# Performance work log

Hardware: AMD Instinct MI355X
Metric: run time of the kernel (lower is better)

Reference implementation:

```python
import jax, jax.numpy as jnp
import numpy as np

B, T, C, J = 2048, 128, 3, 25   # batch, frames, coords, joints
E = 64                          # structure elements (n_elements)


def setup_inputs() -> dict:
    key = jax.random.key(0)
    k1, k2 = jax.random.split(key)
    x = jax.random.normal(k1, (B, T, C, J), dtype=jnp.float32)
    centres = jax.random.uniform(k2, (E, 2), dtype=jnp.float32)
    sharpness = jnp.full((E, 2), 3.0, dtype=jnp.float32)  # torch init: ones*3
    return {"x": x, "centres": centres, "sharpness": sharpness}


def _mst_deaths(Dm):
    """Prim's MST over dense distance matrix Dm [n,n].
    The multiset of MST edge weights equals the finite death times of the
    0-dim Vietoris-Rips persistence diagram (births are all 0)."""
    n = Dm.shape[0]
    in_tree0 = jnp.zeros(n, dtype=bool).at[0].set(True)

    def step(carry, _):
        mind, in_tree = carry
        masked = jnp.where(in_tree, jnp.inf, mind)  # distance from tree to each node
        j = jnp.argmin(masked)
        w = masked[j]                               # weight of edge added to MST
        in_tree = in_tree.at[j].set(True)
        mind = jnp.minimum(mind, Dm[j])
        return (mind, in_tree), w

    (_, _), deaths = jax.lax.scan(step, (Dm[0], in_tree0), None, length=n - 1)
    return deaths  # [n-1]


def reference(x, centres, sharpness):
    # --- dense preprocessing ---
    h = x.mean(1)                           # [B, C, J]
    h = h[..., :, None] - h[..., None, :]   # [B, C, J, J] pairwise coord diffs
    h = h.mean(-3)                          # [B, J, J]
    h = jnp.sqrt((h * h).sum(axis=1))       # torch.norm(., 2, dim=1) -> [B, J]
    lo, hi = h.min(), h.max()
    rng = hi - lo
    safe = rng > 1e-8
    h = jnp.where(safe, (h - lo) / jnp.where(safe, rng, 1.0), jnp.zeros_like(h))

    # --- Vietoris-Rips dim-0 persistence on point cloud h: B points in J dims ---
    sq = (h * h).sum(-1)
    d2 = sq[:, None] + sq[None, :] - 2.0 * (h @ h.T)       # [B, B]
    Dm = jnp.sqrt(jnp.maximum(d2, 1e-12))
    deaths = _mst_deaths(Dm)                               # [B-1]
    pd = jnp.stack([jnp.zeros_like(deaths), deaths], -1)[None]  # [1, P, 2]

    # --- StructureElementLayer: out[b,e] = sum_p exp(-sum_d s[e,d]^2 (pd-c)^2) ---
    s2 = sharpness * sharpness                             # [E, 2]
    diff = pd[:, :, None, :] - centres[None, None, :, :]   # [1, P, E, 2]
    out = jnp.exp(-(diff * diff * s2).sum(-1)).sum(1)      # [1, E]
    return out
```

## Files before the change

kernel.cpp:

```cpp
#include <hip/hip_runtime.h>
#include <math.h>

#define B_N 2048
#define T_N 128
#define C_N 3
#define J_N 25
#define E_N 64
#define TC  (T_N*C_N)
#define TCJ (TC*J_N)
#define NQ4 (TCJ/4)
#define NC  256

#define D_OFF      0
#define H_OFF      (B_N*B_N)
#define BLO_OFF    (H_OFF + B_N*J_N)
#define BHI_OFF    (BLO_OFF + B_N)
#define DEATHS_OFF (BHI_OFF + B_N)
#define BEST_OFF   (DEATHS_OFF + B_N)
#define COMP_OFF   (BEST_OFF + 4*B_N)
#define GC_OFF     (COMP_OFF + 2*B_N)
#define DC_OFF     (GC_OFF + 2)

typedef unsigned long long u64;
#define U64MAX 0xFFFFFFFFFFFFFFFFull
#define U32INF 0xFFFFFFFFu

__global__ void __launch_bounds__(256) k_reduce(const float* __restrict__ x,
                                                float* __restrict__ ws) {
    __shared__ float4 part[250];
    __shared__ float S[100];
    __shared__ float Mj[25];
    const int t = threadIdx.x, b = blockIdx.x;
    const float4* x4 = (const float4*)(x + (size_t)b * TCJ);
    if (t < 250) {
        float4 a; a.x = a.y = a.z = a.w = 0.f;
        for (int idx = t; idx < NQ4; idx += 250) {
            float4 v = x4[idx];
            a.x += v.x; a.y += v.y; a.z += v.z; a.w += v.w;
        }
        part[t] = a;
    }
    __syncthreads();
    if (t < 25) {
        float4 s = part[t];
        #pragma unroll
        for (int g = 1; g < 10; ++g) {
            float4 v = part[t + 25 * g];
            s.x += v.x; s.y += v.y; s.z += v.z; s.w += v.w;
        }
        S[4*t] = s.x; S[4*t+1] = s.y; S[4*t+2] = s.z; S[4*t+3] = s.w;
    }
    __syncthreads();
    if (t < 25) Mj[t] = (S[t] + S[t+25] + S[t+50] + S[t+75]) * (1.0f / 384.0f);
    __syncthreads();
    if (t < 25) {
        float mj = Mj[t], acc = 0.f;
        #pragma unroll
        for (int i = 0; i < J_N; ++i) { float d = Mj[i] - mj; acc += d * d; }
        float hv = sqrtf(acc);
        ws[H_OFF + b * J_N + t] = hv;
        S[t] = hv;
    }
    __syncthreads();
    if (t == 0) {
        float lo = S[0], hi = S[0];
        #pragma unroll
        for (int i = 1; i < J_N; ++i) { lo = fminf(lo, S[i]); hi = fmaxf(hi, S[i]); }
        ws[BLO_OFF + b] = lo;
        ws[BHI_OFF + b] = hi;
    }
}

__global__ void __launch_bounds__(1024) k_distscan(float* __restrict__ ws) {
    __shared__ float A[8][26];
    __shared__ float Bsh[1024 * J_N];
    __shared__ u64 part[16];
    const int t = threadIdx.x, blk = blockIdx.x;
    const int tx = t & 127, grp = t >> 7;
    const float* h = ws + H_OFF;
    const int row0 = blk * 8;
    if (t < 8 * J_N) A[t / J_N][t % J_N] = h[row0 * J_N + t];
    if (blk < 64) ((unsigned*)(ws + DC_OFF))[blk * 1024 + t] = U32INF;
    if (blk == 0) {
        unsigned* gc = (unsigned*)(ws + COMP_OFF);
        gc[t] = (unsigned)t; gc[t + 1024] = (unsigned)(t + 1024);
        if (t == 0) { ((unsigned*)(ws + GC_OFF))[0] = 0u; ((unsigned*)(ws + GC_OFF))[1] = 0u; }
    }
    const int row = row0 + grp;
    float ar[J_N];
    u64 bestk = U64MAX;
    float* D = ws + D_OFF;
    for (int mt = 0; mt < 2; ++mt) {
        __syncthreads();
        for (int idx = t; idx < 1024 * J_N; idx += 1024)
            Bsh[idx] = h[mt * 1024 * J_N + idx];
        __syncthreads();
        if (mt == 0) {
            #pragma unroll
            for (int k = 0; k < J_N; ++k) ar[k] = A[grp][k];
        }
        #pragma unroll 2
        for (int cc = 0; cc < 8; ++cc) {
            const int lcol = cc * 128 + tx;
            const int col = mt * 1024 + lcol;
            const float* bp = &Bsh[lcol * J_N];
            float acc = 0.f;
            #pragma unroll
            for (int k = 0; k < J_N; ++k) { float d = ar[k] - bp[k]; acc += d * d; }
            float dist = sqrtf(fmaxf(acc, 1e-12f));
            D[(size_t)row * B_N + col] = dist;
            if (col != row) {
                unsigned a = min((unsigned)row, (unsigned)col);
                unsigned b2 = max((unsigned)row, (unsigned)col);
                u64 key = ((u64)__float_as_uint(dist) << 32) | (a << 11) | b2;
                if (key < bestk) bestk = key;
            }
        }
    }
    #pragma unroll
    for (int off = 32; off; off >>= 1) {
        u64 o = __shfl_down(bestk, off);
        if (o < bestk) bestk = o;
    }
    if ((t & 63) == 0) part[t >> 6] = bestk;
    __syncthreads();
    if (t < 8) {
        u64 a = part[2 * t], b = part[2 * t + 1];
        ((u64*)(ws + BEST_OFF))[row0 + t] = a < b ? a : b;
    }
}

__global__ void __launch_bounds__(1024) k_round(float* __restrict__ ws, int par_in) {
    unsigned* gcnt = (unsigned*)(ws + GC_OFF);
    const unsigned base = gcnt[par_in];
    if (base >= B_N - 1) return;
    __shared__ __align__(16) unsigned comp[B_N];
    __shared__ u64 cb[B_N];
    __shared__ unsigned par[B_N];
    __shared__ unsigned cnt_s;
    const int t = threadIdx.x, blk = blockIdx.x;
    const unsigned* gcomp_in = (const unsigned*)(ws + COMP_OFF) + par_in * B_N;
    unsigned* gcomp_out = (unsigned*)(ws + COMP_OFF) + (par_in ^ 1) * B_N;
    const u64* bin = (const u64*)(ws + BEST_OFF) + par_in * B_N;
    u64* bout = (u64*)(ws + BEST_OFF) + (par_in ^ 1) * B_N;
    float* deaths = ws + DEATHS_OFF;

    if (t == 0) cnt_s = 0u;
    comp[t] = gcomp_in[t]; comp[t + 1024] = gcomp_in[t + 1024];
    cb[t] = U64MAX; cb[t + 1024] = U64MAX;
    __syncthreads();
    #pragma unroll
    for (int i = t; i < B_N; i += 1024) {
        u64 bk = bin[i];
        if (bk != U64MAX) atomicMin(&cb[comp[i]], bk);
    }
    __syncthreads();
    #pragma unroll
    for (int c = t; c < B_N; c += 1024) {
        u64 k = cb[c];
        unsigned p = (unsigned)c;
        if (k != U64MAX) {
            unsigned a  = (unsigned)((k >> 11) & 0x7FFu);
            unsigned b2 = (unsigned)(k & 0x7FFu);
            unsigned ca = comp[a], cbv = comp[b2];
            unsigned c2 = (ca == (unsigned)c) ? cbv : ca;
            p = c2;
            if (!(cb[c2] == k && c2 < (unsigned)c)) {
                unsigned li = atomicAdd(&cnt_s, 1u);
                if (blk == 0) deaths[base + li] = __uint_as_float((unsigned)(k >> 32));
            }
        }
        par[c] = p;
    }
    __syncthreads();
    #pragma unroll
    for (int c = t; c < B_N; c += 1024) {
        unsigned p = par[c];
        if (p != (unsigned)c && par[p] == (unsigned)c && (unsigned)c < p) par[c] = (unsigned)c;
    }
    __syncthreads();
    #pragma unroll
    for (int c = t; c < B_N; c += 1024) {
        unsigned r = par[c];
        while (true) { unsigned pr = par[r]; if (pr == r) break; r = pr; }
        par[c] = r;
    }
    __syncthreads();
    #pragma unroll
    for (int i = t; i < B_N; i += 1024) comp[i] = par[comp[i]];
    __syncthreads();
    const unsigned newbase = base + cnt_s;
    if (blk == 0) {
        gcomp_out[t] = comp[t]; gcomp_out[t + 1024] = comp[t + 1024];
        if (t == 0) { gcnt[par_in ^ 1] = newbase; if (newbase >= B_N - 1) gcnt[par_in] = newbase; }
    }
    if (newbase >= B_N - 1) return;

    const int w = t >> 6, lane = t & 63;
    if (w >= 8) return;
    const int row = blk * 8 + w;
    const unsigned ci = comp[row];
    u64 prev = bin[row];
    {
        unsigned pa = (unsigned)((prev >> 11) & 0x7FFu);
        unsigned pb = (unsigned)(prev & 0x7FFu);
        unsigned jo = (pa == (unsigned)row) ? pb : pa;
        if (comp[jo] != ci) {
            if (lane == 0) bout[row] = prev;
            return;
        }
    }
    const float4* row4 = (const float4*)(ws + D_OFF + (size_t)row * B_N);
    const uint4* comp4 = (const uint4*)comp;
    u64 best = U64MAX;
    #pragma unroll
    for (int k = 0; k < 8; ++k) {
        const int q = k * 64 + lane;
        float4 w4 = row4[q];
        uint4  c4 = comp4[q];
        const unsigned j0 = (unsigned)(q * 4);
        float wv[4] = {w4.x, w4.y, w4.z, w4.w};
        unsigned cv[4] = {c4.x, c4.y, c4.z, c4.w};
        #pragma unroll
        for (int m = 0; m < 4; ++m) {
            if (cv[m] != ci) {
                unsigned j = j0 + m;
                unsigned a = min((unsigned)row, j), b2 = max((unsigned)row, j);
                u64 key = ((u64)__float_as_uint(wv[m]) << 32) | (a << 11) | b2;
                if (key < best) best = key;
            }
        }
    }
    #pragma unroll
    for (int off = 32; off; off >>= 1) {
        u64 o = __shfl_down(best, off);
        if (o < best) best = o;
    }
    if (lane == 0) bout[row] = best;
}

__global__ void __launch_bounds__(1024) k_round3c(float* __restrict__ ws) {
    unsigned* gcnt = (unsigned*)(ws + GC_OFF);
    const unsigned base = gcnt[0];
    if (base >= B_N - 1) return;
    __shared__ __align__(16) unsigned comp[B_N];
    __shared__ u64 cb[B_N];
    __shared__ unsigned par[B_N];
    __shared__ unsigned cflag[B_N];
    __shared__ unsigned pd[8][NC];
    __shared__ unsigned cnt_s, csum[16];
    const int t = threadIdx.x, blk = blockIdx.x;
    const unsigned* gcomp_in = (const unsigned*)(ws + COMP_OFF);
    const u64* bin = (const u64*)(ws + BEST_OFF);
    float* deaths = ws + DEATHS_OFF;

    if (t == 0) cnt_s = 0u;
    comp[t] = gcomp_in[t]; comp[t + 1024] = gcomp_in[t + 1024];
    cb[t] = U64MAX; cb[t + 1024] = U64MAX;
    __syncthreads();
    #pragma unroll
    for (int i = t; i < B_N; i += 1024) {
        u64 bk = bin[i];
        if (bk != U64MAX) atomicMin(&cb[comp[i]], bk);
    }
    __syncthreads();
    #pragma unroll
    for (int c = t; c < B_N; c += 1024) {
        u64 k = cb[c];
        unsigned p = (unsigned)c;
        if (k != U64MAX) {
            unsigned a  = (unsigned)((k >> 11) & 0x7FFu);
            unsigned b2 = (unsigned)(k & 0x7FFu);
            unsigned ca = comp[a], cbv = comp[b2];
            unsigned c2 = (ca == (unsigned)c) ? cbv : ca;
            p = c2;
            if (!(cb[c2] == k && c2 < (unsigned)c)) {
                unsigned li = atomicAdd(&cnt_s, 1u);
                if (blk == 0) deaths[base + li] = __uint_as_float((unsigned)(k >> 32));
            }
        }
        par[c] = p;
    }
    __syncthreads();
    #pragma unroll
    for (int c = t; c < B_N; c += 1024) {
        unsigned p = par[c];
        if (p != (unsigned)c && par[p] == (unsigned)c && (unsigned)c < p) par[c] = (unsigned)c;
    }
    __syncthreads();
    #pragma unroll
    for (int c = t; c < B_N; c += 1024) {
        unsigned r = par[c];
        while (true) { unsigned pr = par[r]; if (pr == r) break; r = pr; }
        par[c] = r;
    }
    __syncthreads();
    #pragma unroll
    for (int i = t; i < B_N; i += 1024) comp[i] = par[comp[i]];
    __syncthreads();
    const unsigned newbase = base + cnt_s;
    if (blk == 0 && t == 0) { gcnt[0] = newbase; gcnt[1] = newbase; }
    if (newbase >= B_N - 1) return;

    cflag[t] = 0u; cflag[t + 1024] = 0u;
    __syncthreads();
    cflag[comp[t]] = 1u; cflag[comp[t + 1024]] = 1u;
    __syncthreads();
    const unsigned lane = t & 63, w = t >> 6;
    unsigned f0 = cflag[2 * t], f1 = cflag[2 * t + 1];
    unsigned s = f0 + f1, sc = s;
    #pragma unroll
    for (int off = 1; off < 64; off <<= 1) {
        unsigned v = __shfl_up(sc, off);
        if (lane >= (unsigned)off) sc += v;
    }
    if (lane == 63) csum[w] = sc;
    __syncthreads();
    if (t < 16) {
        unsigned v = csum[t], acc = v;
        #pragma unroll
        for (int off = 1; off < 16; off <<= 1) {
            unsigned u2 = __shfl_up(acc, off);
            if (t >= off) acc += u2;
        }
        csum[t] = acc - v;
    }
    __syncthreads();
    unsigned off0 = csum[w] + (sc - s);
    __syncthreads();
    if (f0) cflag[2 * t] = off0;
    if (f1) cflag[2 * t + 1] = off0 + f0;
    __syncthreads();

    #pragma unroll
    for (int i = 0; i < 2; ++i) pd[0][i * 1024 + t] = U32INF;
    __syncthreads();
    const int row = blk * 8 + (int)w;
    unsigned ci = 0u;
    if (w < 8) {
        ci = comp[row];
        const float4* row4 = (const float4*)(ws + D_OFF + (size_t)row * B_N);
        const uint4* comp4 = (const uint4*)comp;
        #pragma unroll
        for (int k = 0; k < 8; ++k) {
            const int q = k * 64 + (int)lane;
            float4 w4 = row4[q];
            uint4  c4 = comp4[q];
            float wv[4] = {w4.x, w4.y, w4.z, w4.w};
            unsigned cv[4] = {c4.x, c4.y, c4.z, c4.w};
            #pragma unroll
            for (int m = 0; m < 4; ++m) {
                if (cv[m] != ci) atomicMin(&pd[w][cflag[cv[m]]], __float_as_uint(wv[m]));
            }
        }
    }
    __syncthreads();
    if (w < 8) {
        unsigned* gDc = (unsigned*)(ws + DC_OFF);
        const unsigned ri = cflag[ci];
        for (int j2 = (int)lane; j2 < NC; j2 += 64) {
            unsigned v = pd[w][j2];
            if (v != U32INF) atomicMin(&gDc[ri * NC + j2], v);
        }
    }
}

__global__ void __launch_bounds__(1024) k_finishstruct(float* __restrict__ ws,
                                                       const float* __restrict__ centres,
                                                       const float* __restrict__ sharp,
                                                       float* __restrict__ out) {
    __shared__ unsigned short Dcs[NC * NC];
    __shared__ u64 cbf[NC];
    __shared__ unsigned parf[NC], ccomp[NC];
    __shared__ unsigned cnt_s, base_s;
    __shared__ float redlo[16], redhi[16];
    const int t = threadIdx.x;
    const int lane = t & 63, w = t >> 6;
    float* deaths = ws + DEATHS_OFF;
    const unsigned base0 = ((const unsigned*)(ws + GC_OFF))[0];

    if (base0 < B_N - 1) {
        const unsigned ncr = (unsigned)B_N - base0;
        const unsigned* gDc = (const unsigned*)(ws + DC_OFF);
        for (unsigned idx = (unsigned)t; idx < ncr * NC; idx += 1024u)
            Dcs[idx] = (unsigned short)(gDc[idx] >> 16);
        if (t < NC) ccomp[t] = (unsigned)t;
        if (t == 0) base_s = base0;
        __syncthreads();
        const int HH = (int)((ncr + 63u) >> 6);
        for (int iter = 0; iter < 8; ++iter) {
            if (t < NC) cbf[t] = U64MAX;
            if (t == 0) cnt_s = 0u;
            __syncthreads();
            for (unsigned r = (unsigned)w; r < ncr; r += 16u) {
                const unsigned cc = ccomp[r];
                u64 key = U64MAX;
                for (int hh = 0; hh < HH; ++hh) {
                    const unsigned c = (unsigned)lane + (unsigned)hh * 64u;
                    unsigned wv = Dcs[r * NC + c];
                    if (wv != 0xFFFFu && ccomp[c] != cc) {
                        unsigned a = min(r, c);
                        unsigned b2 = max(r, c);
                        u64 k2 = ((u64)wv << 32) | (a << 8) | b2;
                        if (k2 < key) key = k2;
                    }
                }
                #pragma unroll
                for (int off = 32; off; off >>= 1) {
                    u64 o = __shfl_down(key, off);
                    if (o < key) key = o;
                }
                if (lane == 0 && key != U64MAX) atomicMin(&cbf[cc], key);
            }
            __syncthreads();
            bool add = false; float dw = 0.f;
            if (t < NC) {
                u64 k = cbf[t];
                unsigned p = (unsigned)t;
                if (k != U64MAX) {
                    unsigned a = (unsigned)((k >> 8) & 255u), b2 = (unsigned)(k & 255u);
                    unsigned ca = ccomp[a], cbv = ccomp[b2];
                    unsigned c2 = (ca == (unsigned)t) ? cbv : ca;
                    p = c2;
                    if (!(cbf[c2] == k && c2 < (unsigned)t)) {
                        add = true;
                        dw = __uint_as_float((unsigned)(k >> 32) << 16);
                    }
                }
                parf[t] = p;
            }
            __syncthreads();
            if (t < NC) {
                unsigned pp = parf[t];
                if (pp != (unsigned)t && parf[pp] == (unsigned)t && (unsigned)t < pp) parf[t] = (unsigned)t;
            }
            __syncthreads();
            if (t < NC) {
                unsigned r2 = parf[t];
                while (parf[r2] != r2) r2 = parf[r2];
                parf[t] = r2;
            }
            __syncthreads();
            if (t < NC) {
                if (add) { unsigned li = atomicAdd(&cnt_s, 1u); deaths[base_s + li] = dw; }
                ccomp[t] = parf[ccomp[t]];
            }
            __syncthreads();
            if (t == 0) base_s += cnt_s;
            __syncthreads();
            if (base_s >= B_N - 1) break;
        }
        __syncthreads();
    }

    float lo = INFINITY, hi = -INFINITY;
    #pragma unroll
    for (int i = t; i < B_N; i += 1024) {
        lo = fminf(lo, ws[BLO_OFF + i]);
        hi = fmaxf(hi, ws[BHI_OFF + i]);
    }
    #pragma unroll
    for (int off = 32; off; off >>= 1) {
        lo = fminf(lo, __shfl_down(lo, off));
        hi = fmaxf(hi, __shfl_down(hi, off));
    }
    if (lane == 0) { redlo[w] = lo; redhi[w] = hi; }
    __syncthreads();
    lo = redlo[0]; hi = redhi[0];
    #pragma unroll
    for (int k = 1; k < 16; ++k) { lo = fminf(lo, redlo[k]); hi = fmaxf(hi, redhi[k]); }
    float rng = hi - lo;
    float rinv = (rng > 1e-8f) ? 1.0f / rng : 0.0f;

    for (int e = w; e < E_N; e += 16) {
        const float c0 = centres[e * 2], c1 = centres[e * 2 + 1];
        const float s0 = sharp[e * 2],   s1 = sharp[e * 2 + 1];
        const float s1sq = s1 * s1;
        float acc = 0.f;
        for (int p = lane; p < B_N - 1; p += 64) {
            float d = deaths[p] * rinv - c1;
            acc += expf(-s1sq * d * d);
        }
        #pragma unroll
        for (int off = 32; off; off >>= 1) acc += __shfl_down(acc, off);
        if (lane == 0) out[e] = expf(-s0 * s0 * c0 * c0) * acc;
    }
}

extern "C" void kernel_launch(void* const* d_in, const int* in_sizes, int n_in,
                              void* d_out, int out_size, void* d_ws, size_t ws_size,
                              hipStream_t stream) {
    const float* x       = (const float*)d_in[0];
    const float* centres = (const float*)d_in[1];
    const float* sharp   = (const float*)d_in[2];
    float* out = (float*)d_out;
    float* ws  = (float*)d_ws;

    hipLaunchKernelGGL(k_reduce,   dim3(B_N),  dim3(256),  0, stream, x, ws);
    hipLaunchKernelGGL(k_distscan, dim3(256),  dim3(1024), 0, stream, ws);
    hipLaunchKernelGGL(k_round,    dim3(256),  dim3(1024), 0, stream, ws, 0);
    hipLaunchKernelGGL(k_round,    dim3(256),  dim3(1024), 0, stream, ws, 1);
    hipLaunchKernelGGL(k_round3c,  dim3(256),  dim3(1024), 0, stream, ws);
    hipLaunchKernelGGL(k_finishstruct, dim3(1), dim3(1024), 0, stream, ws, centres, sharp, out);
}
```

Before: 172.9 us.

## Fuse distance scan and Boruvka rounds into one cooperative kernel with grid sync

Merges the distance/scan kernel, the two Boruvka round kernels and the contraction kernel into a single cooperative kernel that uses grid.sync between phases. The component array stays in shared memory across rounds, so it no longer round-trips through global memory and three kernel launches are removed. Shared memory is overlaid between the distance tile and the round buffers. This requires all 256 blocks of 1024 threads to be co-resident for cooperative launch, and grid.sync has its own cost.

```diff
diff --git a/kernel.cpp b/kernel.cpp
--- a/kernel.cpp
+++ b/kernel.cpp
@@ -1,5 +1,8 @@
 #include <hip/hip_runtime.h>
+#include <hip/hip_cooperative_groups.h>
 #include <math.h>
+
+namespace cg = cooperative_groups;
 
 #define B_N 2048
 #define T_N 128
@@ -71,25 +74,78 @@
     }
 }
 
-__global__ void __launch_bounds__(1024) k_distscan(float* __restrict__ ws) {
+#define UNION_PHASE(binp)                                                     \
+  {                                                                           \
+    if (t == 0) cnt_s = 0u;                                                   \
+    cb[t] = U64MAX; cb[t + 1024] = U64MAX;                                    \
+    __syncthreads();                                                          \
+    for (int i = t; i < B_N; i += 1024) {                                     \
+      u64 bk = (binp)[i];                                                     \
+      if (bk != U64MAX) atomicMin(&cb[comp[i]], bk);                          \
+    }                                                                         \
+    __syncthreads();                                                          \
+    for (int c = t; c < B_N; c += 1024) {                                     \
+      u64 k = cb[c];                                                          \
+      unsigned p = (unsigned)c;                                               \
+      if (k != U64MAX) {                                                      \
+        unsigned a  = (unsigned)((k >> 11) & 0x7FFu);                         \
+        unsigned b2 = (unsigned)(k & 0x7FFu);                                 \
+        unsigned ca = comp[a], cbv = comp[b2];                                \
+        unsigned c2 = (ca == (unsigned)c) ? cbv : ca;                         \
+        p = c2;                                                               \
+        if (!(cb[c2] == k && c2 < (unsigned)c)) {                             \
+          unsigned li = atomicAdd(&cnt_s, 1u);                                \
+          if (blk == 0) deaths[curbase + li] = __uint_as_float((unsigned)(k >> 32)); \
+        }                                                                     \
+      }                                                                       \
+      par[c] = p;                                                             \
+    }                                                                         \
+    __syncthreads();                                                          \
+    for (int c = t; c < B_N; c += 1024) {                                     \
+      unsigned p = par[c];                                                    \
+      if (p != (unsigned)c && par[p] == (unsigned)c && (unsigned)c < p) par[c] = (unsigned)c; \
+    }                                                                         \
+    __syncthreads();                                                          \
+    for (int c = t; c < B_N; c += 1024) {                                     \
+      unsigned r2 = par[c];                                                   \
+      while (true) { unsigned pr = par[r2]; if (pr == r2) break; r2 = pr; }   \
+      par[c] = r2;                                                            \
+    }                                                                         \
+    __syncthreads();                                                          \
+    for (int i = t; i < B_N; i += 1024) comp[i] = par[comp[i]];               \
+    __syncthreads();                                                          \
+    curbase += cnt_s;                                                         \
+    __syncthreads();                                                          \
+  }
+
+__global__ void __launch_bounds__(1024) k_coop(float* __restrict__ ws) {
+    cg::grid_group grid = cg::this_grid();
     __shared__ float A[8][26];
-    __shared__ float Bsh[1024 * J_N];
     __shared__ u64 part[16];
+    __shared__ __align__(16) unsigned comp[B_N];
+    __shared__ unsigned cnt_s, csum[16];
+    __shared__ __align__(16) char ovl[1024 * J_N * 4];
+    u64*      cb    = (u64*)ovl;
+    unsigned* par   = (unsigned*)(ovl + 16384);
+    unsigned* cflag = (unsigned*)(ovl + 24576);
+    unsigned* pd    = (unsigned*)(ovl + 32768);
+    float*    Bsh   = (float*)ovl;
+
     const int t = threadIdx.x, blk = blockIdx.x;
+    const int lane = t & 63, w = t >> 6;
+    const float* h = ws + H_OFF;
+    float* deaths = ws + DEATHS_OFF;
+    u64* BEST = (u64*)(ws + BEST_OFF);
+    float* D = ws + D_OFF;
+
     const int tx = t & 127, grp = t >> 7;
-    const float* h = ws + H_OFF;
     const int row0 = blk * 8;
     if (t < 8 * J_N) A[t / J_N][t % J_N] = h[row0 * J_N + t];
     if (blk < 64) ((unsigned*)(ws + DC_OFF))[blk * 1024 + t] = U32INF;
-    if (blk == 0) {
-        unsigned* gc = (unsigned*)(ws + COMP_OFF);
-        gc[t] = (unsigned)t; gc[t + 1024] = (unsigned)(t + 1024);
-        if (t == 0) { ((unsigned*)(ws + GC_OFF))[0] = 0u; ((unsigned*)(ws + GC_OFF))[1] = 0u; }
-    }
-    const int row = row0 + grp;
+    comp[t] = (unsigned)t; comp[t + 1024] = (unsigned)(t + 1024);
+    const int srow = row0 + grp;
     float ar[J_N];
     u64 bestk = U64MAX;
-    float* D = ws + D_OFF;
     for (int mt = 0; mt < 2; ++mt) {
         __syncthreads();
         for (int idx = t; idx < 1024 * J_N; idx += 1024)
@@ -108,10 +164,10 @@
             #pragma unroll
             for (int k = 0; k < J_N; ++k) { float d = ar[k] - bp[k]; acc += d * d; }
             float dist = sqrtf(fmaxf(acc, 1e-12f));
-            D[(size_t)row * B_N + col] = dist;
-            if (col != row) {
-                unsigned a = min((unsigned)row, (unsigned)col);
-                unsigned b2 = max((unsigned)row, (unsigned)col);
+            D[(size_t)srow * B_N + col] = dist;
+            if (col != srow) {
+                unsigned a = min((unsigned)srow, (unsigned)col);
+                unsigned b2 = max((unsigned)srow, (unsigned)col);
                 u64 key = ((u64)__float_as_uint(dist) << 32) | (a << 11) | b2;
                 if (key < bestk) bestk = key;
             }
@@ -126,193 +182,83 @@
     __syncthreads();
     if (t < 8) {
         u64 a = part[2 * t], b = part[2 * t + 1];
-        ((u64*)(ws + BEST_OFF))[row0 + t] = a < b ? a : b;
-    }
-}
-
-__global__ void __launch_bounds__(1024) k_round(float* __restrict__ ws, int par_in) {
-    unsigned* gcnt = (unsigned*)(ws + GC_OFF);
-    const unsigned base = gcnt[par_in];
-    if (base >= B_N - 1) return;
-    __shared__ __align__(16) unsigned comp[B_N];
-    __shared__ u64 cb[B_N];
-    __shared__ unsigned par[B_N];
-    __shared__ unsigned cnt_s;
-    const int t = threadIdx.x, blk = blockIdx.x;
-    const unsigned* gcomp_in = (const unsigned*)(ws + COMP_OFF) + par_in * B_N;
-    unsigned* gcomp_out = (unsigned*)(ws + COMP_OFF) + (par_in ^ 1) * B_N;
-    const u64* bin = (const u64*)(ws + BEST_OFF) + par_in * B_N;
-    u64* bout = (u64*)(ws + BEST_OFF) + (par_in ^ 1) * B_N;
-    float* deaths = ws + DEATHS_OFF;
-
-    if (t == 0) cnt_s = 0u;
-    comp[t] = gcomp_in[t]; comp[t + 1024] = gcomp_in[t + 1024];
-    cb[t] = U64MAX; cb[t + 1024] = U64MAX;
-    __syncthreads();
-    #pragma unroll
-    for (int i = t; i < B_N; i += 1024) {
-        u64 bk = bin[i];
-        if (bk != U64MAX) atomicMin(&cb[comp[i]], bk);
-    }
-    __syncthreads();
-    #pragma unroll
-    for (int c = t; c < B_N; c += 1024) {
-        u64 k = cb[c];
-        unsigned p = (unsigned)c;
-        if (k != U64MAX) {
-            unsigned a  = (unsigned)((k >> 11) & 0x7FFu);
-            unsigned b2 = (unsigned)(k & 0x7FFu);
-            unsigned ca = comp[a], cbv = comp[b2];
-            unsigned c2 = (ca == (unsigned)c) ? cbv : ca;
-            p = c2;
-            if (!(cb[c2] == k && c2 < (unsigned)c)) {
-                unsigned li = atomicAdd(&cnt_s, 1u);
-                if (blk == 0) deaths[base + li] = __uint_as_float((unsigned)(k >> 32));
-            }
-        }
-        par[c] = p;
-    }
-    __syncthreads();
-    #pragma unroll
-    for (int c = t; c < B_N; c += 1024) {
-        unsigned p = par[c];
-        if (p != (unsigned)c && par[p] == (unsigned)c && (unsigned)c < p) par[c] = (unsigned)c;
-    }
-    __syncthreads();
-    #pragma unroll
-    for (int c = t; c < B_N; c += 1024) {
-        unsigned r = par[c];
-        while (true) { unsigned pr = par[r]; if (pr == r) break; r = pr; }
-        par[c] = r;
-    }
-    __syncthreads();
-    #pragma unroll
-    for (int i = t; i < B_N; i += 1024) comp[i] = par[comp[i]];
-    __syncthreads();
-    const unsigned newbase = base + cnt_s;
-    if (blk == 0) {
-        gcomp_out[t] = comp[t]; gcomp_out[t + 1024] = comp[t + 1024];
-        if (t == 0) { gcnt[par_in ^ 1] = newbase; if (newbase >= B_N - 1) gcnt[par_in] = newbase; }
-    }
-    if (newbase >= B_N - 1) return;
-
-    const int w = t >> 6, lane = t & 63;
-    if (w >= 8) return;
-    const int row = blk * 8 + w;
-    const unsigned ci = comp[row];
-    u64 prev = bin[row];
-    {
-        unsigned pa = (unsigned)((prev >> 11) & 0x7FFu);
-        unsigned pb = (unsigned)(prev & 0x7FFu);
-        unsigned jo = (pa == (unsigned)row) ? pb : pa;
-        if (comp[jo] != ci) {
-            if (lane == 0) bout[row] = prev;
-            return;
-        }
-    }
-    const float4* row4 = (const float4*)(ws + D_OFF + (size_t)row * B_N);
-    const uint4* comp4 = (const uint4*)comp;
-    u64 best = U64MAX;
-    #pragma unroll
-    for (int k = 0; k < 8; ++k) {
-        const int q = k * 64 + lane;
-        float4 w4 = row4[q];
-        uint4  c4 = comp4[q];
-        const unsigned j0 = (unsigned)(q * 4);
-        float wv[4] = {w4.x, w4.y, w4.z, w4.w};
-        unsigned cv[4] = {c4.x, c4.y, c4.z, c4.w};
-        #pragma unroll
-        for (int m = 0; m < 4; ++m) {
-            if (cv[m] != ci) {
-                unsigned j = j0 + m;
-                unsigned a = min((unsigned)row, j), b2 = max((unsigned)row, j);
-                u64 key = ((u64)__float_as_uint(wv[m]) << 32) | (a << 11) | b2;
-                if (key < best) best = key;
-            }
-        }
-    }
-    #pragma unroll
-    for (int off = 32; off; off >>= 1) {
-        u64 o = __shfl_down(best, off);
-        if (o < best) best = o;
-    }
-    if (lane == 0) bout[row] = best;
-}
-
-__global__ void __launch_bounds__(1024) k_round3c(float* __restrict__ ws) {
-    unsigned* gcnt = (unsigned*)(ws + GC_OFF);
-    const unsigned base = gcnt[0];
-    if (base >= B_N - 1) return;
-    __shared__ __align__(16) unsigned comp[B_N];
-    __shared__ u64 cb[B_N];
-    __shared__ unsigned par[B_N];
-    __shared__ unsigned cflag[B_N];
-    __shared__ unsigned pd[8][NC];
-    __shared__ unsigned cnt_s, csum[16];
-    const int t = threadIdx.x, blk = blockIdx.x;
-    const unsigned* gcomp_in = (const unsigned*)(ws + COMP_OFF);
-    const u64* bin = (const u64*)(ws + BEST_OFF);
-    float* deaths = ws + DEATHS_OFF;
-
-    if (t == 0) cnt_s = 0u;
-    comp[t] = gcomp_in[t]; comp[t + 1024] = gcomp_in[t + 1024];
-    cb[t] = U64MAX; cb[t + 1024] = U64MAX;
-    __syncthreads();
-    #pragma unroll
-    for (int i = t; i < B_N; i += 1024) {
-        u64 bk = bin[i];
-        if (bk != U64MAX) atomicMin(&cb[comp[i]], bk);
-    }
-    __syncthreads();
-    #pragma unroll
-    for (int c = t; c < B_N; c += 1024) {
-        u64 k = cb[c];
-        unsigned p = (unsigned)c;
-        if (k != U64MAX) {
-            unsigned a  = (unsigned)((k >> 11) & 0x7FFu);
-            unsigned b2 = (unsigned)(k & 0x7FFu);
-            unsigned ca = comp[a], cbv = comp[b2];
-            unsigned c2 = (ca == (unsigned)c) ? cbv : ca;
-            p = c2;
-            if (!(cb[c2] == k && c2 < (unsigned)c)) {
-                unsigned li = atomicAdd(&cnt_s, 1u);
-                if (blk == 0) deaths[base + li] = __uint_as_float((unsigned)(k >> 32));
-            }
-        }
-        par[c] = p;
-    }
-    __syncthreads();
-    #pragma unroll
-    for (int c = t; c < B_N; c += 1024) {
-        unsigned p = par[c];
-        if (p != (unsigned)c && par[p] == (unsigned)c && (unsigned)c < p) par[c] = (unsigned)c;
-    }
-    __syncthreads();
-    #pragma unroll
-    for (int c = t; c < B_N; c += 1024) {
-        unsigned r = par[c];
-        while (true) { unsigned pr = par[r]; if (pr == r) break; r = pr; }
-        par[c] = r;
-    }
-    __syncthreads();
-    #pragma unroll
-    for (int i = t; i < B_N; i += 1024) comp[i] = par[comp[i]];
-    __syncthreads();
-    const unsigned newbase = base + cnt_s;
-    if (blk == 0 && t == 0) { gcnt[0] = newbase; gcnt[1] = newbase; }
-    if (newbase >= B_N - 1) return;
+        BEST[row0 + t] = a < b ? a : b;
+    }
+    __threadfence();
+    grid.sync();
+
+    unsigned curbase = 0u;
+    bool done = false;
+    for (int r = 0; r < 2; ++r) {
+        const u64* bin = BEST + (r & 1) * B_N;
+        u64* bout = BEST + ((r & 1) ^ 1) * B_N;
+        if (!done) {
+            UNION_PHASE(bin);
+            if (curbase >= B_N - 1) {
+                done = true;
+            } else if (w < 8) {
+                const int row = blk * 8 + w;
+                const unsigned ci = comp[row];
+                u64 prev = bin[row];
+                unsigned pa = (unsigned)((prev >> 11) & 0x7FFu);
+                unsigned pb = (unsigned)(prev & 0x7FFu);
+                unsigned jo = (pa == (unsigned)row) ? pb : pa;
+                if (comp[jo] != ci) {
+                    if (lane == 0) bout[row] = prev;
+                } else {
+                    const float4* row4 = (const float4*)(D + (size_t)row * B_N);
+                    const uint4* comp4 = (const uint4*)comp;
+                    u64 best = U64MAX;
+                    #pragma unroll
+                    for (int k = 0; k < 8; ++k) {
+                        const int q = k * 64 + lane;
+                        float4 w4 = row4[q];
+                        uint4  c4 = comp4[q];
+                        const unsigned j0 = (unsigned)(q * 4);
+                        float wv[4] = {w4.x, w4.y, w4.z, w4.w};
+                        unsigned cv[4] = {c4.x, c4.y, c4.z, c4.w};
+                        #pragma unroll
+                        for (int m = 0; m < 4; ++m) {
+                            if (cv[m] != ci) {
+                                unsigned j = j0 + m;
+                                unsigned a = min((unsigned)row, j), b2 = max((unsigned)row, j);
+                                u64 key = ((u64)__float_as_uint(wv[m]) << 32) | (a << 11) | b2;
+                                if (key < best) best = key;
+                            }
+                        }
+                    }
+                    #pragma unroll
+                    for (int off = 32; off; off >>= 1) {
+                        u64 o = __shfl_down(best, off);
+                        if (o < best) best = o;
+                    }
+                    if (lane == 0) bout[row] = best;
+                }
+            }
+        }
+        __threadfence();
+        grid.sync();
+    }
+
+    if (!done) {
+        UNION_PHASE(BEST);
+    }
+    if (blk == 0 && t == 0) {
+        unsigned* gcnt = (unsigned*)(ws + GC_OFF);
+        gcnt[0] = curbase; gcnt[1] = curbase;
+    }
+    if (curbase >= B_N - 1) return;
 
     cflag[t] = 0u; cflag[t + 1024] = 0u;
     __syncthreads();
     cflag[comp[t]] = 1u; cflag[comp[t + 1024]] = 1u;
     __syncthreads();
-    const unsigned lane = t & 63, w = t >> 6;
     unsigned f0 = cflag[2 * t], f1 = cflag[2 * t + 1];
     unsigned s = f0 + f1, sc = s;
     #pragma unroll
     for (int off = 1; off < 64; off <<= 1) {
         unsigned v = __shfl_up(sc, off);
-        if (lane >= (unsigned)off) sc += v;
+        if (lane >= off) sc += v;
     }
     if (lane == 63) csum[w] = sc;
     __syncthreads();
@@ -332,34 +278,33 @@
     if (f1) cflag[2 * t + 1] = off0 + f0;
     __syncthreads();
 
-    #pragma unroll
-    for (int i = 0; i < 2; ++i) pd[0][i * 1024 + t] = U32INF;
-    __syncthreads();
-    const int row = blk * 8 + (int)w;
-    unsigned ci = 0u;
+    pd[t] = U32INF; pd[t + 1024] = U32INF;
+    __syncthreads();
+    const int crow = blk * 8 + w;
+    unsigned ci2 = 0u;
     if (w < 8) {
-        ci = comp[row];
-        const float4* row4 = (const float4*)(ws + D_OFF + (size_t)row * B_N);
+        ci2 = comp[crow];
+        const float4* row4 = (const float4*)(D + (size_t)crow * B_N);
         const uint4* comp4 = (const uint4*)comp;
         #pragma unroll
         for (int k = 0; k < 8; ++k) {
-            const int q = k * 64 + (int)lane;
+            const int q = k * 64 + lane;
             float4 w4 = row4[q];
             uint4  c4 = comp4[q];
             float wv[4] = {w4.x, w4.y, w4.z, w4.w};
             unsigned cv[4] = {c4.x, c4.y, c4.z, c4.w};
             #pragma unroll
             for (int m = 0; m < 4; ++m) {
-                if (cv[m] != ci) atomicMin(&pd[w][cflag[cv[m]]], __float_as_uint(wv[m]));
+                if (cv[m] != ci2) atomicMin(&pd[w * NC + cflag[cv[m]]], __float_as_uint(wv[m]));
             }
         }
     }
     __syncthreads();
     if (w < 8) {
         unsigned* gDc = (unsigned*)(ws + DC_OFF);
-        const unsigned ri = cflag[ci];
-        for (int j2 = (int)lane; j2 < NC; j2 += 64) {
-            unsigned v = pd[w][j2];
+        const unsigned ri = cflag[ci2];
+        for (int j2 = lane; j2 < NC; j2 += 64) {
+            unsigned v = pd[w * NC + j2];
             if (v != U32INF) atomicMin(&gDc[ri * NC + j2], v);
         }
     }
@@ -496,10 +441,9 @@
     float* out = (float*)d_out;
     float* ws  = (float*)d_ws;
 
-    hipLaunchKernelGGL(k_reduce,   dim3(B_N),  dim3(256),  0, stream, x, ws);
-    hipLaunchKernelGGL(k_distscan, dim3(256),  dim3(1024), 0, stream, ws);
-    hipLaunchKernelGGL(k_round,    dim3(256),  dim3(1024), 0, stream, ws, 0);
-    hipLaunchKernelGGL(k_round,    dim3(256),  dim3(1024), 0, stream, ws, 1);
-    hipLaunchKernelGGL(k_round3c,  dim3(256),  dim3(1024), 0, stream, ws);
+    hipLaunchKernelGGL(k_reduce, dim3(B_N), dim3(256), 0, stream, x, ws);
+    void* cargs[] = { (void*)&ws };
+    hipLaunchCooperativeKernel((const void*)k_coop, dim3(256), dim3(1024),
+                               cargs, 0, stream);
     hipLaunchKernelGGL(k_finishstruct, dim3(1), dim3(1024), 0, stream, ws, centres, sharp, out);
 }
```

Measured after the change: 471.4 us. 173% more time.
